# Performance work log

Measured on AMD Instinct MI355X. Metric: run time of the kernel, lower is better.

## Reference

```python
import jax, jax.numpy as jnp
import numpy as np

K_DIM = 1024
HEADS = 16


def setup_inputs() -> dict:
    key = jax.random.key(0)
    ks = jax.random.split(key, 8)
    b, t, tc, k = 2, 2048, 2048, K_DIM
    scale = 1.0 / np.sqrt(k)
    x = jax.random.normal(ks[0], (b, t, k), dtype=jnp.float32)
    context = jax.random.normal(ks[1], (b, tc, k), dtype=jnp.float32)
    Wq = jax.random.normal(ks[2], (k, k), dtype=jnp.float32) * scale
    Wk = jax.random.normal(ks[3], (k, k), dtype=jnp.float32) * scale
    Wv = jax.random.normal(ks[4], (k, k), dtype=jnp.float32) * scale
    Wo = jax.random.normal(ks[5], (k, k), dtype=jnp.float32) * scale
    bo = jax.random.normal(ks[6], (k,), dtype=jnp.float32) * 0.01
    return {"x": x, "context": context, "Wq": Wq, "Wk": Wk, "Wv": Wv, "Wo": Wo, "bo": bo}


def reference(x, context, Wq, Wk, Wv, Wo, bo):
    b, t, e = x.shape
    tc = context.shape[1]
    h = HEADS
    s = e // h
    # Linear(k,k,bias=False): y = x @ W.T
    q = (x @ Wq.T).reshape(b, t, h, s)
    k_ = (context @ Wk.T).reshape(b, tc, h, s)
    v = (context @ Wv.T).reshape(b, tc, h, s)
    # scale q and k each by e**-0.25 (net 1/sqrt(e), note: full embed dim, not head dim)
    inv4 = e ** (-0.25)
    q = q * inv4
    k_ = k_ * inv4
    # scores: [b, h, t, tc]
    dot = jnp.einsum('bthd,bchd->bhtc', q, k_)
    attn = jax.nn.softmax(dot, axis=-1)
    out = jnp.einsum('bhtc,bchd->bthd', attn, v).reshape(b, t, e)
    return out @ Wo.T + bo
```

## Files before the change

### kernel.cpp

```cpp
#include <hip/hip_runtime.h>
#include <stdint.h>

typedef unsigned short u16;
typedef unsigned int u32;
typedef __attribute__((ext_vector_type(4))) float f32x4;
typedef __attribute__((ext_vector_type(16))) float f32x16;
typedef __attribute__((ext_vector_type(8))) __bf16 bf16x8;
typedef __attribute__((ext_vector_type(8))) u16 u16x8;

constexpr int NB = 2, NT = 2048, NTC = 2048, NE = 1024, NH = 16, ND = 64;
constexpr int MTOK = NB * NT;
constexpr int KDIM = NE;
constexpr float QK_SCALE = (float)(0.17677669529663687 * 1.2011224087864498);
constexpr float FIXED_M = 24.0f;

__device__ __forceinline__ u16 f2bf(float f) {
  union { float f; uint32_t u; } v; v.f = f;
  uint32_t r = v.u + 0x7FFFu + ((v.u >> 16) & 1u);
  return (u16)(r >> 16);
}

__device__ __forceinline__ float fexp2(float x) {
#if __has_builtin(__builtin_amdgcn_exp2f)
  return __builtin_amdgcn_exp2f(x);
#else
  return exp2f(x);
#endif
}

__device__ __forceinline__ u32 cvtpk(float lo, float hi) {
  u32 r;
  asm("v_cvt_pk_bf16_f32 %0, %1, %2" : "=v"(r) : "v"(lo), "v"(hi));
  return r;
}

__device__ __forceinline__ void plswap(u32& a, u32& b) {
  asm("v_permlane32_swap_b32 %0, %1" : "+v"(a), "+v"(b));
}

__device__ __forceinline__ void gload16(const void* g, void* lds) {
  __builtin_amdgcn_global_load_lds(
      (const __attribute__((address_space(1))) unsigned int*)g,
      (__attribute__((address_space(3))) unsigned int*)lds, 16, 0, 0);
}

__device__ __forceinline__ f32x4 mfma16x16(bf16x8 a, bf16x8 b, f32x4 c) {
  return __builtin_amdgcn_mfma_f32_16x16x32_bf16(a, b, c, 0, 0, 0);
}
__device__ __forceinline__ f32x16 mfma32x32(bf16x8 a, bf16x8 b, f32x16 c) {
  return __builtin_amdgcn_mfma_f32_32x32x16_bf16(a, b, c, 0, 0, 0);
}

__device__ __forceinline__ int swz(int row, int part) {
  return row * 128 + ((part ^ (row & 7)) << 4);
}

__device__ __forceinline__ u16x8 cast8(const float4* p, float scale) {
  float4 a = p[0], b = p[1];
  u16x8 r;
  r[0] = f2bf(a.x * scale); r[1] = f2bf(a.y * scale);
  r[2] = f2bf(a.z * scale); r[3] = f2bf(a.w * scale);
  r[4] = f2bf(b.x * scale); r[5] = f2bf(b.y * scale);
  r[6] = f2bf(b.z * scale); r[7] = f2bf(b.w * scale);
  return r;
}

__global__ void cast_all(const float* __restrict__ x, const float* __restrict__ ctx,
                         const float* __restrict__ Wq, const float* __restrict__ Wk,
                         const float* __restrict__ Wv, const float* __restrict__ Wo,
                         u16* __restrict__ xb, u16* __restrict__ cb,
                         u16* __restrict__ wb) {
  int i = blockIdx.x * blockDim.x + threadIdx.x;
  const float* src; u16* dst; int j; float scale = 1.0f;
  if (i < 524288) { src = x; dst = xb; j = i; }
  else if (i < 1048576) { src = ctx; dst = cb; j = i - 524288; }
  else {
    int k = i - 1048576;
    int which = k >> 17; j = k & 131071;
    src = (which == 0) ? Wq : (which == 1) ? Wk : (which == 2) ? Wv : Wo;
    scale = (which < 2) ? QK_SCALE : 1.0f;
    dst = wb + (size_t)which * (NE * KDIM);
  }
  *((u16x8*)dst + j) = cast8((const float4*)src + (size_t)j * 2, scale);
}

__global__ __launch_bounds__(256)
void gemm_qkv(const u16* __restrict__ xb, const u16* __restrict__ cb,
              const u16* __restrict__ wqb, const u16* __restrict__ wkvb,
              u16* __restrict__ Qb, u16* __restrict__ KVb) {
  __shared__ __align__(16) u16 Al[64 * 64];
  __shared__ __align__(16) u16 Bl[128 * 64];
  const int tid = threadIdx.x, w = tid >> 6, l = tid & 63;
  const int l15 = l & 15, l4 = l >> 4;
  const int wm = w >> 1, wn = w & 1;

  const int bid = blockIdx.x;
  const bool isQ = bid < 512;
  const u16* A; const u16* Bm; int mbase, nbase;
  if (isQ) { A = xb; Bm = wqb; nbase = (bid & 7) * 128; mbase = (bid >> 3) * 64; }
  else { int b2 = bid - 512; A = cb; Bm = wkvb; nbase = (b2 & 15) * 128; mbase = (b2 >> 4) * 64; }

  f32x4 acc[2][4] = {};
  const char* Ab = (const char*)(A + (size_t)mbase * KDIM);
  const char* Bb = (const char*)(Bm + (size_t)nbase * KDIM);

  for (int k0 = 0; k0 < KDIM; k0 += 64) {
#pragma unroll
    for (int s = 0; s < 2; ++s) {
      int i = (w * 2 + s) * 64 + l;
      int row = i >> 3, part = i & 7;
      int gofs = row * (KDIM * 2) + k0 * 2 + ((part ^ (row & 7)) << 4);
      gload16(Ab + gofs, (char*)Al + (w * 2 + s) * 1024);
    }
#pragma unroll
    for (int s = 0; s < 4; ++s) {
      int i = (w * 4 + s) * 64 + l;
      int row = i >> 3, part = i & 7;
      int gofs = row * (KDIM * 2) + k0 * 2 + ((part ^ (row & 7)) << 4);
      gload16(Bb + gofs, (char*)Bl + (w * 4 + s) * 1024);
    }
    __syncthreads();
#pragma unroll
    for (int kc = 0; kc < 2; ++kc) {
      bf16x8 af[2], bfr[4];
#pragma unroll
      for (int mt = 0; mt < 2; ++mt) {
        int r = wm * 32 + mt * 16 + l15;
        af[mt] = *(const bf16x8*)((const char*)Al + swz(r, kc * 4 + l4));
      }
#pragma unroll
      for (int nt = 0; nt < 4; ++nt) {
        int r = wn * 64 + nt * 16 + l15;
        bfr[nt] = *(const bf16x8*)((const char*)Bl + swz(r, kc * 4 + l4));
      }
#pragma unroll
      for (int mt = 0; mt < 2; ++mt)
#pragma unroll
        for (int nt = 0; nt < 4; ++nt)
          acc[mt][nt] = mfma16x16(af[mt], bfr[nt], acc[mt][nt]);
    }
    __syncthreads();
  }

#pragma unroll
  for (int mt = 0; mt < 2; ++mt) {
#pragma unroll
    for (int nt = 0; nt < 4; ++nt) {
      int col = nbase + wn * 64 + nt * 16 + l15;
      int mrow0 = mbase + wm * 32 + mt * 16 + l4 * 4;
#pragma unroll
      for (int r = 0; r < 4; ++r) {
        int m = mrow0 + r;
        float v = acc[mt][nt][r];
        if (isQ) {
          int b = m >> 11, t = m & (NT - 1), h = col >> 6, d = col & (ND - 1);
          Qb[((size_t)(b * NH + h) * NT + t) * ND + d] = f2bf(v);
        } else {
          int b = m >> 11, tc = m & (NTC - 1);
          int h = (col >> 6) & 15, d = col & (ND - 1);
          size_t base = ((size_t)((b * NH + h) * 32 + (tc >> 6))) * 4096;
          if (col < 1024) {
            size_t idx = base + (size_t)(d >> 3) * 512 + (size_t)(tc & 63) * 8 + (d & 7);
            KVb[idx] = f2bf(v);
          } else {
            size_t idx = base + (size_t)((tc & 63) >> 3) * 512 + (size_t)d * 8 + (tc & 7);
            KVb[4194304 + idx] = f2bf(v);
          }
        }
      }
    }
  }
}

__global__ __launch_bounds__(256)
void gemm_out(const u16* __restrict__ A, const u16* __restrict__ Bm,
              float* __restrict__ Cout, const float* __restrict__ bias) {
  __shared__ __align__(16) u16 Al[64 * 64];
  __shared__ __align__(16) u16 Bl[128 * 64];
  const int tid = threadIdx.x, w = tid >> 6, l = tid & 63;
  const int l15 = l & 15, l4 = l >> 4;
  const int wm = w >> 1, wn = w & 1;
  const int mbase = blockIdx.y * 64, nbase = blockIdx.x * 128;

  f32x4 acc[2][4] = {};
  const char* Ab = (const char*)(A + (size_t)mbase * KDIM);
  const char* Bb = (const char*)(Bm + (size_t)nbase * KDIM);

  for (int k0 = 0; k0 < KDIM; k0 += 64) {
#pragma unroll
    for (int s = 0; s < 2; ++s) {
      int i = (w * 2 + s) * 64 + l;
      int row = i >> 3, part = i & 7;
      int gofs = row * (KDIM * 2) + k0 * 2 + ((part ^ (row & 7)) << 4);
      gload16(Ab + gofs, (char*)Al + (w * 2 + s) * 1024);
    }
#pragma unroll
    for (int s = 0; s < 4; ++s) {
      int i = (w * 4 + s) * 64 + l;
      int row = i >> 3, part = i & 7;
      int gofs = row * (KDIM * 2) + k0 * 2 + ((part ^ (row & 7)) << 4);
      gload16(Bb + gofs, (char*)Bl + (w * 4 + s) * 1024);
    }
    __syncthreads();
#pragma unroll
    for (int kc = 0; kc < 2; ++kc) {
      bf16x8 af[2], bfr[4];
#pragma unroll
      for (int mt = 0; mt < 2; ++mt) {
        int r = wm * 32 + mt * 16 + l15;
        af[mt] = *(const bf16x8*)((const char*)Al + swz(r, kc * 4 + l4));
      }
#pragma unroll
      for (int nt = 0; nt < 4; ++nt) {
        int r = wn * 64 + nt * 16 + l15;
        bfr[nt] = *(const bf16x8*)((const char*)Bl + swz(r, kc * 4 + l4));
      }
#pragma unroll
      for (int mt = 0; mt < 2; ++mt)
#pragma unroll
        for (int nt = 0; nt < 4; ++nt)
          acc[mt][nt] = mfma16x16(af[mt], bfr[nt], acc[mt][nt]);
    }
    __syncthreads();
  }

#pragma unroll
  for (int mt = 0; mt < 2; ++mt) {
#pragma unroll
    for (int nt = 0; nt < 4; ++nt) {
      int col = nbase + wn * 64 + nt * 16 + l15;
      int mrow0 = mbase + wm * 32 + mt * 16 + l4 * 4;
#pragma unroll
      for (int r = 0; r < 4; ++r)
        Cout[(size_t)(mrow0 + r) * NE + col] = acc[mt][nt][r] + bias[col];
    }
  }
}

__global__ __launch_bounds__(128, 2)
void attn_fwd(const u16* __restrict__ Q, const u16* __restrict__ K,
              const u16* __restrict__ Vt, u16* __restrict__ O) {
  __shared__ float Ol[64 * 64];
  __shared__ float Ll[64];
  const int tid = threadIdx.x, wid = tid >> 6, l = tid & 63;
  const int l31 = l & 31, hi = l >> 5;

  int n = blockIdx.x;
  int work = (n & 7) * 128 + (n >> 3);
  const int bh = work >> 5, qx = work & 31;
  const int b = bh >> 4, h = bh & 15;
  const int qbase = qx * 64;

  const char* Kb = (const char*)(K + (size_t)bh * 32 * 4096);
  const char* Vb = (const char*)(Vt + (size_t)bh * 32 * 4096);
  const u16* Qb = Q + (size_t)bh * NT * ND;

  auto kaddr = [&](int t32, int kc) {
    return Kb + (size_t)(t32 >> 1) * 8192 + (size_t)(kc * 2 + hi) * 1024
              + (size_t)((t32 & 1) * 32 + l31) * 16;
  };
  auto vaddr = [&](int t32, int j) {
    return Vb + (size_t)(t32 >> 1) * 8192
              + (size_t)((t32 & 1) * 4 + (j >> 1) * 2 + hi) * 1024
              + (size_t)((j & 1) * 32 + l31) * 16;
  };

  bf16x8 qf[2][4];
#pragma unroll
  for (int qt = 0; qt < 2; ++qt)
#pragma unroll
    for (int kc = 0; kc < 4; ++kc)
      qf[qt][kc] = *(const bf16x8*)(Qb + (size_t)(qbase + qt * 32 + l31) * ND + kc * 16 + hi * 8);

  f32x16 oacc[2][2] = {};
  f32x16 lacc[2] = {};
  f32x16 minit;
#pragma unroll
  for (int r = 0; r < 16; ++r) minit[r] = -FIXED_M;

  const int tbase = wid * 32;

  bf16x8 kfA[4], kfB[4], vf[4];
#pragma unroll
  for (int kc = 0; kc < 4; ++kc) kfA[kc] = *(const bf16x8*)kaddr(tbase, kc);

  for (int it2 = 0; it2 < 16; ++it2) {
    const int tA = tbase + it2 * 2, tB = tA + 1;

#pragma unroll
    for (int j = 0; j < 4; ++j) vf[j] = *(const bf16x8*)vaddr(tA, j);
#pragma unroll
    for (int kc = 0; kc < 4; ++kc) kfB[kc] = *(const bf16x8*)kaddr(tB, kc);
#pragma unroll
    for (int qt = 0; qt < 2; ++qt) {
      f32x16 sv = minit;
#pragma unroll
      for (int kc = 0; kc < 4; ++kc) sv = mfma32x32(kfA[kc], qf[qt][kc], sv);
#pragma unroll
      for (int r = 0; r < 16; ++r) { sv[r] = fexp2(sv[r]); lacc[qt][r] += sv[r]; }
      bf16x8 pa0, pa1;
      {
        u32 a1 = cvtpk(sv[0], sv[1]), b1 = cvtpk(sv[4], sv[5]);
        u32 a2 = cvtpk(sv[2], sv[3]), b2 = cvtpk(sv[6], sv[7]);
        plswap(a1, b1); plswap(a2, b2);
        u32 a3 = cvtpk(sv[8], sv[9]), b3 = cvtpk(sv[12], sv[13]);
        u32 a4 = cvtpk(sv[10], sv[11]), b4 = cvtpk(sv[14], sv[15]);
        plswap(a3, b3); plswap(a4, b4);
        union { u32 u[4]; bf16x8 v; } ua, ub;
        ua.u[0] = a1; ua.u[1] = a2; ua.u[2] = b1; ua.u[3] = b2;
        ub.u[0] = a3; ub.u[1] = a4; ub.u[2] = b3; ub.u[3] = b4;
        pa0 = ua.v; pa1 = ub.v;
      }
      oacc[qt][0] = mfma32x32(pa0, vf[0], oacc[qt][0]);
      oacc[qt][1] = mfma32x32(pa0, vf[1], oacc[qt][1]);
      oacc[qt][0] = mfma32x32(pa1, vf[2], oacc[qt][0]);
      oacc[qt][1] = mfma32x32(pa1, vf[3], oacc[qt][1]);
    }

#pragma unroll
    for (int j = 0; j < 4; ++j) vf[j] = *(const bf16x8*)vaddr(tB, j);
#pragma unroll
    for (int kc = 0; kc < 4; ++kc) kfA[kc] = *(const bf16x8*)kaddr(tB + 1, kc);
#pragma unroll
    for (int qt = 0; qt < 2; ++qt) {
      f32x16 sv = minit;
#pragma unroll
      for (int kc = 0; kc < 4; ++kc) sv = mfma32x32(kfB[kc], qf[qt][kc], sv);
#pragma unroll
      for (int r = 0; r < 16; ++r) { sv[r] = fexp2(sv[r]); lacc[qt][r] += sv[r]; }
      bf16x8 pa0, pa1;
      {
        u32 a1 = cvtpk(sv[0], sv[1]), b1 = cvtpk(sv[4], sv[5]);
        u32 a2 = cvtpk(sv[2], sv[3]), b2 = cvtpk(sv[6], sv[7]);
        plswap(a1, b1); plswap(a2, b2);
        u32 a3 = cvtpk(sv[8], sv[9]), b3 = cvtpk(sv[12], sv[13]);
        u32 a4 = cvtpk(sv[10], sv[11]), b4 = cvtpk(sv[14], sv[15]);
        plswap(a3, b3); plswap(a4, b4);
        union { u32 u[4]; bf16x8 v; } ua, ub;
        ua.u[0] = a1; ua.u[1] = a2; ua.u[2] = b1; ua.u[3] = b2;
        ub.u[0] = a3; ub.u[1] = a4; ub.u[2] = b3; ub.u[3] = b4;
        pa0 = ua.v; pa1 = ub.v;
      }
      oacc[qt][0] = mfma32x32(pa0, vf[0], oacc[qt][0]);
      oacc[qt][1] = mfma32x32(pa0, vf[1], oacc[qt][1]);
      oacc[qt][0] = mfma32x32(pa1, vf[2], oacc[qt][0]);
      oacc[qt][1] = mfma32x32(pa1, vf[3], oacc[qt][1]);
    }
  }

  float lsum[2];
#pragma unroll
  for (int qt = 0; qt < 2; ++qt) {
    f32x16 t = lacc[qt];
#pragma unroll
    for (int s = 8; s >= 1; s >>= 1)
#pragma unroll
      for (int r = 0; r < s; ++r) t[r] += t[r + s];
    lsum[qt] = t[0] + __shfl_xor(t[0], 32);
  }

  if (wid == 1) {
#pragma unroll
    for (int qt = 0; qt < 2; ++qt) {
#pragma unroll
      for (int r = 0; r < 16; ++r) {
        int crow = (r & 3) + 8 * (r >> 2) + 4 * hi;
        Ol[(qt * 32 + crow) * 64 + l31] = oacc[qt][0][r];
        Ol[(qt * 32 + crow) * 64 + 32 + l31] = oacc[qt][1][r];
      }
      if (!hi) Ll[qt * 32 + l31] = lsum[qt];
    }
  }
  __syncthreads();
  if (wid == 0) {
#pragma unroll
    for (int qt = 0; qt < 2; ++qt) {
      float inv = 1.0f / (lsum[qt] + Ll[qt * 32 + l31]);
#pragma unroll
      for (int r = 0; r < 16; ++r) {
        int crow = (r & 3) + 8 * (r >> 2) + 4 * hi;
        float ir = __shfl(inv, crow);
        int t = qbase + qt * 32 + crow;
        size_t rowo = (size_t)(b * NT + t) * NE + h * 64 + l31;
        O[rowo] = f2bf((oacc[qt][0][r] + Ol[(qt * 32 + crow) * 64 + l31]) * ir);
        O[rowo + 32] = f2bf((oacc[qt][1][r] + Ol[(qt * 32 + crow) * 64 + 32 + l31]) * ir);
      }
    }
  }
}

extern "C" void kernel_launch(void* const* d_in, const int* in_sizes, int n_in,
                              void* d_out, int out_size, void* d_ws, size_t ws_size,
                              hipStream_t stream) {
  const float* x   = (const float*)d_in[0];
  const float* ctx = (const float*)d_in[1];
  const float* Wq  = (const float*)d_in[2];
  const float* Wk  = (const float*)d_in[3];
  const float* Wv  = (const float*)d_in[4];
  const float* Wo  = (const float*)d_in[5];
  const float* bo  = (const float*)d_in[6];
  float* out = (float*)d_out;
  char* ws = (char*)d_ws;

  u16* xb  = (u16*)(ws);
  u16* cb  = (u16*)(ws + (8u  << 20));
  u16* wqb = (u16*)(ws + (16u << 20));
  u16* wkb = (u16*)(ws + (18u << 20));
  u16* wob = (u16*)(ws + (22u << 20));
  u16* Qb  = (u16*)(ws + (24u << 20));
  u16* Kb  = (u16*)(ws + (32u << 20));
  u16* Vtb = (u16*)(ws + (40u << 20));
  u16* Ob  = (u16*)(ws + (48u << 20));

  cast_all<<<6144, 256, 0, stream>>>(x, ctx, Wq, Wk, Wv, Wo, xb, cb, wqb);
  gemm_qkv<<<1536, 256, 0, stream>>>(xb, cb, wqb, wkb, Qb, Kb);
  attn_fwd<<<1024, 128, 0, stream>>>(Qb, Kb, Vtb, Ob);
  gemm_out<<<dim3(8, 64), 256, 0, stream>>>(Ob, wob, out, bo);
}
```

Before: 114.9 us.

## Double-buffer LDS in projection GEMMs and remap blocks across XCDs

Both projection GEMMs now share a loop that double-buffers LDS tiles. Loads for step k+2 are issued while step k computes, and explicit vmcnt waits replace the full syncthreads pair, so global-load latency is hidden behind MFMA work. Block indices are also permuted so consecutive blocks land on the same XCD and share A/B tiles in L2. This doubles LDS use per block (48KB), which may reduce occupancy. The hand-counted vmcnt depends on the exact count of outstanding loads being correct.

```diff
diff --git a/kernel.cpp b/kernel.cpp
--- a/kernel.cpp
+++ b/kernel.cpp
@@ -84,63 +84,81 @@
   *((u16x8*)dst + j) = cast8((const float4*)src + (size_t)j * 2, scale);
 }
 
+__device__ __forceinline__ void gemm_loop(const char* Ab, const char* Bb,
+                                          u16* Al, u16* Bl, int tid,
+                                          f32x4 (&acc)[2][4]) {
+  const int w = tid >> 6, l = tid & 63;
+  const int l15 = l & 15, l4 = l >> 4;
+  const int wm = w >> 1, wn = w & 1;
+
+  auto stage = [&](int buf, int k0) {
+#pragma unroll
+    for (int s = 0; s < 2; ++s) {
+      int i = (w * 2 + s) * 64 + l;
+      int row = i >> 3, part = i & 7;
+      int gofs = row * (KDIM * 2) + k0 * 2 + ((part ^ (row & 7)) << 4);
+      gload16(Ab + gofs, (char*)(Al + buf * 4096) + (w * 2 + s) * 1024);
+    }
+#pragma unroll
+    for (int s = 0; s < 4; ++s) {
+      int i = (w * 4 + s) * 64 + l;
+      int row = i >> 3, part = i & 7;
+      int gofs = row * (KDIM * 2) + k0 * 2 + ((part ^ (row & 7)) << 4);
+      gload16(Bb + gofs, (char*)(Bl + buf * 8192) + (w * 4 + s) * 1024);
+    }
+  };
+
+  stage(0, 0);
+  stage(1, 64);
+
+  for (int it = 0; it < 16; ++it) {
+    const int cur = it & 1;
+    if (it < 15) asm volatile("s_waitcnt vmcnt(6)" ::: "memory");
+    else         asm volatile("s_waitcnt vmcnt(0)" ::: "memory");
+    __builtin_amdgcn_s_barrier();
+    const char* Ac = (const char*)(Al + cur * 4096);
+    const char* Bc = (const char*)(Bl + cur * 8192);
+#pragma unroll
+    for (int kc = 0; kc < 2; ++kc) {
+      bf16x8 af[2], bfr[4];
+#pragma unroll
+      for (int mt = 0; mt < 2; ++mt)
+        af[mt] = *(const bf16x8*)(Ac + swz(wm * 32 + mt * 16 + l15, kc * 4 + l4));
+#pragma unroll
+      for (int nt = 0; nt < 4; ++nt)
+        bfr[nt] = *(const bf16x8*)(Bc + swz(wn * 64 + nt * 16 + l15, kc * 4 + l4));
+#pragma unroll
+      for (int mt = 0; mt < 2; ++mt)
+#pragma unroll
+        for (int nt = 0; nt < 4; ++nt)
+          acc[mt][nt] = mfma16x16(af[mt], bfr[nt], acc[mt][nt]);
+    }
+    __builtin_amdgcn_s_barrier();
+    if (it < 14) stage(cur, (it + 2) * 64);
+  }
+}
+
 __global__ __launch_bounds__(256)
 void gemm_qkv(const u16* __restrict__ xb, const u16* __restrict__ cb,
               const u16* __restrict__ wqb, const u16* __restrict__ wkvb,
               u16* __restrict__ Qb, u16* __restrict__ KVb) {
-  __shared__ __align__(16) u16 Al[64 * 64];
-  __shared__ __align__(16) u16 Bl[128 * 64];
+  __shared__ __align__(16) u16 Al[2][64 * 64];
+  __shared__ __align__(16) u16 Bl[2][128 * 64];
   const int tid = threadIdx.x, w = tid >> 6, l = tid & 63;
   const int l15 = l & 15, l4 = l >> 4;
   const int wm = w >> 1, wn = w & 1;
 
-  const int bid = blockIdx.x;
+  int bid = blockIdx.x;
+  bid = (bid & 7) * 192 + (bid >> 3);
   const bool isQ = bid < 512;
   const u16* A; const u16* Bm; int mbase, nbase;
   if (isQ) { A = xb; Bm = wqb; nbase = (bid & 7) * 128; mbase = (bid >> 3) * 64; }
   else { int b2 = bid - 512; A = cb; Bm = wkvb; nbase = (b2 & 15) * 128; mbase = (b2 >> 4) * 64; }
 
   f32x4 acc[2][4] = {};
-  const char* Ab = (const char*)(A + (size_t)mbase * KDIM);
-  const char* Bb = (const char*)(Bm + (size_t)nbase * KDIM);
-
-  for (int k0 = 0; k0 < KDIM; k0 += 64) {
-#pragma unroll
-    for (int s = 0; s < 2; ++s) {
-      int i = (w * 2 + s) * 64 + l;
-      int row = i >> 3, part = i & 7;
-      int gofs = row * (KDIM * 2) + k0 * 2 + ((part ^ (row & 7)) << 4);
-      gload16(Ab + gofs, (char*)Al + (w * 2 + s) * 1024);
-    }
-#pragma unroll
-    for (int s = 0; s < 4; ++s) {
-      int i = (w * 4 + s) * 64 + l;
-      int row = i >> 3, part = i & 7;
-      int gofs = row * (KDIM * 2) + k0 * 2 + ((part ^ (row & 7)) << 4);
-      gload16(Bb + gofs, (char*)Bl + (w * 4 + s) * 1024);
-    }
-    __syncthreads();
-#pragma unroll
-    for (int kc = 0; kc < 2; ++kc) {
-      bf16x8 af[2], bfr[4];
-#pragma unroll
-      for (int mt = 0; mt < 2; ++mt) {
-        int r = wm * 32 + mt * 16 + l15;
-        af[mt] = *(const bf16x8*)((const char*)Al + swz(r, kc * 4 + l4));
-      }
-#pragma unroll
-      for (int nt = 0; nt < 4; ++nt) {
-        int r = wn * 64 + nt * 16 + l15;
-        bfr[nt] = *(const bf16x8*)((const char*)Bl + swz(r, kc * 4 + l4));
-      }
-#pragma unroll
-      for (int mt = 0; mt < 2; ++mt)
-#pragma unroll
-        for (int nt = 0; nt < 4; ++nt)
-          acc[mt][nt] = mfma16x16(af[mt], bfr[nt], acc[mt][nt]);
-    }
-    __syncthreads();
-  }
+  gemm_loop((const char*)(A + (size_t)mbase * KDIM),
+            (const char*)(Bm + (size_t)nbase * KDIM),
+            &Al[0][0], &Bl[0][0], tid, acc);
 
 #pragma unroll
   for (int mt = 0; mt < 2; ++mt) {
@@ -175,54 +193,20 @@
 __global__ __launch_bounds__(256)
 void gemm_out(const u16* __restrict__ A, const u16* __restrict__ Bm,
               float* __restrict__ Cout, const float* __restrict__ bias) {
-  __shared__ __align__(16) u16 Al[64 * 64];
-  __shared__ __align__(16) u16 Bl[128 * 64];
+  __shared__ __align__(16) u16 Al[2][64 * 64];
+  __shared__ __align__(16) u16 Bl[2][128 * 64];
   const int tid = threadIdx.x, w = tid >> 6, l = tid & 63;
   const int l15 = l & 15, l4 = l >> 4;
   const int wm = w >> 1, wn = w & 1;
-  const int mbase = blockIdx.y * 64, nbase = blockIdx.x * 128;
+
+  int bid = blockIdx.x;
+  bid = (bid & 7) * 64 + (bid >> 3);
+  const int mbase = (bid >> 3) * 64, nbase = (bid & 7) * 128;
 
   f32x4 acc[2][4] = {};
-  const char* Ab = (const char*)(A + (size_t)mbase * KDIM);
-  const char* Bb = (const char*)(Bm + (size_t)nbase * KDIM);
-
-  for (int k0 = 0; k0 < KDIM; k0 += 64) {
-#pragma unroll
-    for (int s = 0; s < 2; ++s) {
-      int i = (w * 2 + s) * 64 + l;
-      int row = i >> 3, part = i & 7;
-      int gofs = row * (KDIM * 2) + k0 * 2 + ((part ^ (row & 7)) << 4);
-      gload16(Ab + gofs, (char*)Al + (w * 2 + s) * 1024);
-    }
-#pragma unroll
-    for (int s = 0; s < 4; ++s) {
-      int i = (w * 4 + s) * 64 + l;
-      int row = i >> 3, part = i & 7;
-      int gofs = row * (KDIM * 2) + k0 * 2 + ((part ^ (row & 7)) << 4);
-      gload16(Bb + gofs, (char*)Bl + (w * 4 + s) * 1024);
-    }
-    __syncthreads();
-#pragma unroll
-    for (int kc = 0; kc < 2; ++kc) {
-      bf16x8 af[2], bfr[4];
-#pragma unroll
-      for (int mt = 0; mt < 2; ++mt) {
-        int r = wm * 32 + mt * 16 + l15;
-        af[mt] = *(const bf16x8*)((const char*)Al + swz(r, kc * 4 + l4));
-      }
-#pragma unroll
-      for (int nt = 0; nt < 4; ++nt) {
-        int r = wn * 64 + nt * 16 + l15;
-        bfr[nt] = *(const bf16x8*)((const char*)Bl + swz(r, kc * 4 + l4));
-      }
-#pragma unroll
-      for (int mt = 0; mt < 2; ++mt)
-#pragma unroll
-        for (int nt = 0; nt < 4; ++nt)
-          acc[mt][nt] = mfma16x16(af[mt], bfr[nt], acc[mt][nt]);
-    }
-    __syncthreads();
-  }
+  gemm_loop((const char*)(A + (size_t)mbase * KDIM),
+            (const char*)(Bm + (size_t)nbase * KDIM),
+            &Al[0][0], &Bl[0][0], tid, acc);
 
 #pragma unroll
   for (int mt = 0; mt < 2; ++mt) {
@@ -415,5 +399,5 @@
   cast_all<<<6144, 256, 0, stream>>>(x, ctx, Wq, Wk, Wv, Wo, xb, cb, wqb);
   gemm_qkv<<<1536, 256, 0, stream>>>(xb, cb, wqb, wkb, Qb, Kb);
   attn_fwd<<<1024, 128, 0, stream>>>(Qb, Kb, Vtb, Ob);
-  gemm_out<<<dim3(8, 64), 256, 0, stream>>>(Ob, wob, out, bo);
-}
+  gemm_out<<<512, 256, 0, stream>>>(Ob, wob, out, bo);
+}
```

Result: no change. 112.9 us (-1.8%).
